# Kernel tuning notes

Hardware: AMD Instinct MI355X
Metric: run time of the kernel (lower is better)

The kernel has to match this reference:

```python
import jax, jax.numpy as jnp
import numpy as np

NOPE, ROPE, LORA, VDIM = 128, 64, 512, 128
T, H, S = 1024, 16, 8192
NUM_CHUNKS = 4  # prefix chunks merged via online-softmax LSE combine
SCALING = (NOPE + ROPE) ** -0.5


def setup_inputs() -> dict:
    key = jax.random.key(0)
    k1, k2, k3, k4 = jax.random.split(key, 4)
    q = jax.random.normal(k1, (T, H, NOPE + ROPE), dtype=jnp.float32)
    kv_cache = jax.random.normal(k2, (S, LORA + ROPE), dtype=jnp.float32)  # latent KV cache [S, 576]
    w_kc = jax.random.normal(k3, (H, NOPE, LORA), dtype=jnp.float32) * (NOPE ** -0.5)
    w_vc = jax.random.normal(k4, (H, LORA, VDIM), dtype=jnp.float32) * (LORA ** -0.5)
    return {"q": q, "kv_cache": kv_cache, "w_kc": w_kc, "w_vc": w_vc}


def _chunk_attn(q_full, kv):
    # q_full: [T,H,576], kv chunk: [C,576] (MQA: single latent KV head)
    scores = jnp.einsum('thd,sd->ths', q_full, kv) * SCALING
    lse = jax.nn.logsumexp(scores, axis=-1)               # [T,H]
    p = jnp.exp(scores - lse[..., None])                  # [T,H,C]
    out = jnp.einsum('ths,sl->thl', p, kv[:, :LORA])      # value = latent kv_lora part
    return out, lse


def reference(q, kv_cache, w_kc, w_vc):
    # --- weight-absorbed query projection (forward_absorb) ---
    q_nope, q_pe = q[..., :NOPE], q[..., NOPE:]
    q_lora = jnp.einsum('thn,hnl->thl', q_nope, w_kc)     # bmm(q_nope^T, w_kc)
    q_full = jnp.concatenate([q_lora, q_pe], axis=-1)     # [T,H,576]

    # --- chunked MQA over latent cache with LSE merge (merge_state_v2) ---
    chunks = kv_cache.reshape(NUM_CHUNKS, S // NUM_CHUNKS, LORA + ROPE)
    acc_out, acc_lse = _chunk_attn(q_full, chunks[0])

    def merge(carry, kv):
        a_out, a_lse = carry
        o, lse = _chunk_attn(q_full, kv)
        new_lse = jnp.logaddexp(a_lse, lse)
        new_out = (a_out * jnp.exp(a_lse - new_lse)[..., None]
                   + o * jnp.exp(lse - new_lse)[..., None])
        return (new_out, new_lse), None

    (attn_out, _), _ = jax.lax.scan(merge, (acc_out, acc_lse), chunks[1:])

    # --- weight-absorbed value projection: bmm(attn^T, w_vc) ---
    out = jnp.einsum('thl,hlv->thv', attn_out, w_vc)      # [T,H,128]
    return out.reshape(T, H * VDIM)
```

## Files before the change

### kernel.cpp

```cpp
#include <hip/hip_runtime.h>
#include <stdint.h>
#include <stddef.h>

#define T_TOK 1024
#define NH    16
#define S_KV  8192
#define DQK   576
#define DV    512
#define NROWS (T_TOK*NH)
#define SCALING 0.072168783648703220563f
#define M_FIX 8.0f

#define SC 32
#define NT (S_KV/SC)
#define KV_CH (72*SC)
#define VT_CH (4*DV)

typedef __attribute__((ext_vector_type(8))) short bf16x8;
typedef __attribute__((ext_vector_type(4))) float f32x4;

__device__ __forceinline__ uint16_t f2bf(float f) {
  uint32_t u = __float_as_uint(f);
  u += 0x7FFFu + ((u >> 16) & 1u);
  return (uint16_t)(u >> 16);
}
__device__ __forceinline__ uint32_t pk2(float a, float b) {
  return (uint32_t)f2bf(a) | ((uint32_t)f2bf(b) << 16);
}
__device__ __forceinline__ void async16(void* lds, const void* g) {
  __builtin_amdgcn_global_load_lds((const __attribute__((address_space(1))) void*)g,
                                   (__attribute__((address_space(3))) void*)lds, 16, 0, 0);
}

__global__ __launch_bounds__(256) void prep_all(
    const float* __restrict__ q, const float* __restrict__ w_kc,
    const float* __restrict__ kv, const float* __restrict__ w_vc,
    uint16_t* __restrict__ q_full, uint16_t* __restrict__ kv_t,
    uint16_t* __restrict__ vt_t, uint16_t* __restrict__ wvt) {
  const int b = blockIdx.x, tid = threadIdx.x;
  __shared__ float qn[32][128];

  if (b < 512) {
    const int h = b >> 5, t0 = (b & 31) * 32;
    #pragma unroll
    for (int r = 0; r < 4; ++r) {
      int idx4 = r * 256 + tid;
      int row = idx4 >> 5, c4 = (idx4 & 31) * 4;
      const float4 v = *(const float4*)(q + ((size_t)((t0 + row) * NH + h)) * 192 + c4);
      *(float4*)&qn[row][c4] = v;
    }
    __syncthreads();
    const int ty = tid >> 6, tx = tid & 63;
    float acc[8][8];
    #pragma unroll
    for (int i = 0; i < 8; ++i)
      #pragma unroll
      for (int j = 0; j < 8; ++j) acc[i][j] = 0.f;
    for (int n = 0; n < 128; ++n) {
      const float4 b0 = *(const float4*)(w_kc + ((size_t)(h * 128 + n)) * 512 + tx * 8);
      const float4 b1 = *(const float4*)(w_kc + ((size_t)(h * 128 + n)) * 512 + tx * 8 + 4);
      #pragma unroll
      for (int i = 0; i < 8; ++i) {
        const float a = qn[ty * 8 + i][n];
        acc[i][0] += a * b0.x; acc[i][1] += a * b0.y; acc[i][2] += a * b0.z; acc[i][3] += a * b0.w;
        acc[i][4] += a * b1.x; acc[i][5] += a * b1.y; acc[i][6] += a * b1.z; acc[i][7] += a * b1.w;
      }
    }
    #pragma unroll
    for (int i = 0; i < 8; ++i) {
      const size_t R = (size_t)(t0 + ty * 8 + i) * NH + h;
      uint4 o;
      o.x = pk2(acc[i][0]*SCALING, acc[i][1]*SCALING);
      o.y = pk2(acc[i][2]*SCALING, acc[i][3]*SCALING);
      o.z = pk2(acc[i][4]*SCALING, acc[i][5]*SCALING);
      o.w = pk2(acc[i][6]*SCALING, acc[i][7]*SCALING);
      *(uint4*)&q_full[R * DQK + tx * 8] = o;
    }
    {
      const int trow = tid >> 3, j0 = (tid & 7) * 8;
      const float* src = q + ((size_t)((t0 + trow) * NH + h)) * 192 + 128 + j0;
      const float4 a = *(const float4*)(src);
      const float4 c = *(const float4*)(src + 4);
      const size_t R = (size_t)(t0 + trow) * NH + h;
      uint4 o;
      o.x = pk2(a.x*SCALING, a.y*SCALING); o.y = pk2(a.z*SCALING, a.w*SCALING);
      o.z = pk2(c.x*SCALING, c.y*SCALING); o.w = pk2(c.z*SCALING, c.w*SCALING);
      *(uint4*)&q_full[R * DQK + 512 + j0] = o;
    }
  } else if (b < 768) {
    const int st = b - 512;
    uint16_t* kvo = kv_t + (size_t)st * (KV_CH * 8);
    #pragma unroll
    for (int r = 0; r < 9; ++r) {
      const int k = r * 256 + tid;
      const int dc = k >> 5, sl = k & 31;
      const float* src = kv + ((size_t)(st * SC + sl)) * DQK + dc * 8;
      const float4 a = *(const float4*)src;
      const float4 c = *(const float4*)(src + 4);
      uint4 o;
      o.x = pk2(a.x, a.y); o.y = pk2(a.z, a.w); o.z = pk2(c.x, c.y); o.w = pk2(c.z, c.w);
      *(uint4*)&kvo[(size_t)k * 8] = o;
    }
    uint16_t* vto = vt_t + (size_t)st * (VT_CH * 8);
    #pragma unroll
    for (int r = 0; r < 8; ++r) {
      const int k = r * 256 + tid;
      const int sc = k >> 9, v = k & 511;
      float val[8];
      #pragma unroll
      for (int e = 0; e < 8; ++e)
        val[e] = kv[((size_t)(st * SC + sc * 8 + e)) * DQK + v];
      uint4 o;
      o.x = pk2(val[0], val[1]); o.y = pk2(val[2], val[3]);
      o.z = pk2(val[4], val[5]); o.w = pk2(val[6], val[7]);
      *(uint4*)&vto[(size_t)k * 8] = o;
    }
  } else {
    const int c = (b - 768) * 256 + tid;
    const int h = c >> 13, rem = c & 8191;
    const int lc = rem >> 7, v = rem & 127;
    const float* src = w_vc + ((size_t)h * 512 + lc * 8) * 128 + v;
    float val[8];
    #pragma unroll
    for (int e = 0; e < 8; ++e) val[e] = src[e * 128];
    uint4 o;
    o.x = pk2(val[0], val[1]); o.y = pk2(val[2], val[3]);
    o.z = pk2(val[4], val[5]); o.w = pk2(val[6], val[7]);
    *(uint4*)&wvt[(size_t)c * 8] = o;
  }
}

__global__ __launch_bounds__(768, 3) void attn_kernel(
    const uint16_t* __restrict__ q_full, const uint16_t* __restrict__ kv_t,
    const uint16_t* __restrict__ vt_t, uint16_t* __restrict__ attn_o) {
  __shared__ short kv_lds[2][KV_CH * 8];
  __shared__ short P_lds[2][260 * 8];
  __shared__ float l_sh[64];

  const int tid = threadIdx.x;
  const int wv = tid >> 6, lane = tid & 63;
  const int cc = lane & 15, quad = lane >> 4;
  const int R0 = blockIdx.x * 64;

  if (wv < 4) {
    const int qh = wv;
    bf16x8 qf[18];
    {
      const uint16_t* qrow = q_full + (size_t)(R0 + 16 * qh + cc) * DQK + quad * 8;
      #pragma unroll
      for (int kk = 0; kk < 18; ++kk)
        qf[kk] = *(const bf16x8*)(qrow + kk * 32);
    }
    const int e = cc & 7, scb = cc >> 3;
    const int qb0 = 16 * qh + quad * 4;

    for (int st = 0; st <= NT; ++st) {
      __syncthreads();
      if (st < NT) {
        const short* kb = kv_lds[st & 1];
        f32x4 sa0 = {0.f,0.f,0.f,0.f}, sa1 = {0.f,0.f,0.f,0.f};
        __builtin_amdgcn_s_setprio(1);
        #pragma unroll
        for (int kk = 0; kk < 18; ++kk) {
          const bf16x8 b0 = *(const bf16x8*)&kb[((kk * 4 + quad) * SC + cc) * 8];
          const bf16x8 b1 = *(const bf16x8*)&kb[((kk * 4 + quad) * SC + 16 + cc) * 8];
          sa0 = __builtin_amdgcn_mfma_f32_16x16x32_bf16(qf[kk], b0, sa0, 0, 0, 0);
          sa1 = __builtin_amdgcn_mfma_f32_16x16x32_bf16(qf[kk], b1, sa1, 0, 0, 0);
        }
        __builtin_amdgcn_s_setprio(0);
        short* Pb = P_lds[st & 1];
        #pragma unroll
        for (int r = 0; r < 4; ++r) {
          Pb[(scb * 65 + qb0 + r) * 8 + e]       = (short)f2bf(__expf(sa0[r] - M_FIX));
          Pb[((2 + scb) * 65 + qb0 + r) * 8 + e] = (short)f2bf(__expf(sa1[r] - M_FIX));
        }
      }
    }
    __syncthreads();
  } else {
    const int ci = wv - 4;
    f32x4 acc[4][4];
    #pragma unroll
    for (int a = 0; a < 4; ++a)
      #pragma unroll
      for (int b = 0; b < 4; ++b) acc[a][b] = (f32x4){0.f, 0.f, 0.f, 0.f};
    f32x4 accl[4];
    #pragma unroll
    for (int a = 0; a < 4; ++a) accl[a] = (f32x4){0.f, 0.f, 0.f, 0.f};
    bf16x8 ones;
    #pragma unroll
    for (int e2 = 0; e2 < 8; ++e2) ones[e2] = (short)0x3F80;

    {
      const uint16_t* kt = kv_t;
      #pragma unroll
      for (int r = 0; r < 5; ++r) {
        const int base = r * 512 + ci * 64;
        if (base < KV_CH)
          async16(&kv_lds[0][base * 8], kt + (size_t)(base + lane) * 8);
      }
    }

    for (int st = 0; st <= NT; ++st) {
      __syncthreads();
      bf16x8 vt4[4];
      if (st > 0) {
        const uint16_t* vtile = vt_t + (size_t)(st - 1) * (VT_CH * 8);
        #pragma unroll
        for (int vj = 0; vj < 4; ++vj)
          vt4[vj] = *(const bf16x8*)(vtile + (size_t)(quad * 512 + 64 * ci + 16 * vj + cc) * 8);
      }
      if (st + 1 < NT) {
        const uint16_t* kt = kv_t + (size_t)(st + 1) * (KV_CH * 8);
        short* dst = kv_lds[(st + 1) & 1];
        #pragma unroll
        for (int r = 0; r < 5; ++r) {
          const int base = r * 512 + ci * 64;
          if (base < KV_CH)
            async16(&dst[base * 8], kt + (size_t)(base + lane) * 8);
        }
      }
      if (st > 0) {
        const short* Pb = P_lds[(st - 1) & 1];
        bf16x8 af[4];
        #pragma unroll
        for (int q2 = 0; q2 < 4; ++q2)
          af[q2] = *(const bf16x8*)&Pb[(quad * 65 + 16 * q2 + cc) * 8];
        __builtin_amdgcn_s_setprio(1);
        if (ci == 0) {
          #pragma unroll
          for (int q2 = 0; q2 < 4; ++q2)
            accl[q2] = __builtin_amdgcn_mfma_f32_16x16x32_bf16(af[q2], ones, accl[q2], 0, 0, 0);
        }
        #pragma unroll
        for (int q2 = 0; q2 < 4; ++q2)
          #pragma unroll
          for (int vj = 0; vj < 4; ++vj)
            acc[q2][vj] = __builtin_amdgcn_mfma_f32_16x16x32_bf16(af[q2], vt4[vj], acc[q2][vj], 0, 0, 0);
        __builtin_amdgcn_s_setprio(0);
      }
    }
    if (ci == 0 && cc == 0) {
      #pragma unroll
      for (int q2 = 0; q2 < 4; ++q2)
        #pragma unroll
        for (int r = 0; r < 4; ++r)
          l_sh[16 * q2 + quad * 4 + r] = accl[q2][r];
    }
    __syncthreads();
    #pragma unroll
    for (int q2 = 0; q2 < 4; ++q2) {
      #pragma unroll
      for (int r = 0; r < 4; ++r) {
        const int row = 16 * q2 + quad * 4 + r;
        const float li = 1.0f / l_sh[row];
        #pragma unroll
        for (int vj = 0; vj < 4; ++vj)
          attn_o[(size_t)(R0 + row) * DV + 64 * ci + 16 * vj + cc] = f2bf(acc[q2][vj][r] * li);
      }
    }
  }
}

__global__ __launch_bounds__(256) void out_proj(const uint16_t* __restrict__ attn_o,
                                                const uint16_t* __restrict__ wvt,
                                                float* __restrict__ out) {
  const int h = blockIdx.y, t0 = blockIdx.x * 64;
  const int wv = threadIdx.x >> 6, lane = threadIdx.x & 63;
  const int cc = lane & 15, quad = lane >> 4;

  f32x4 acc[8];
  #pragma unroll
  for (int vj = 0; vj < 8; ++vj) acc[vj] = (f32x4){0.f, 0.f, 0.f, 0.f};

  const uint16_t* arow = attn_o + ((size_t)(t0 + wv * 16 + cc) * NH + h) * DV + quad * 8;
  const uint16_t* wb = wvt + (size_t)h * (64 * 128) * 8;
  #pragma unroll 4
  for (int kk = 0; kk < 16; ++kk) {
    const bf16x8 a = *(const bf16x8*)(arow + kk * 32);
    #pragma unroll
    for (int vj = 0; vj < 8; ++vj) {
      const bf16x8 b = *(const bf16x8*)(wb + (size_t)(((kk * 4 + quad) * 128) + 16 * vj + cc) * 8);
      acc[vj] = __builtin_amdgcn_mfma_f32_16x16x32_bf16(a, b, acc[vj], 0, 0, 0);
    }
  }
  #pragma unroll
  for (int vj = 0; vj < 8; ++vj)
    #pragma unroll
    for (int r = 0; r < 4; ++r)
      out[(size_t)(t0 + wv * 16 + quad * 4 + r) * (NH * 128) + h * 128 + 16 * vj + cc] = acc[vj][r];
}

extern "C" void kernel_launch(void* const* d_in, const int* in_sizes, int n_in,
                              void* d_out, int out_size, void* d_ws, size_t ws_size,
                              hipStream_t stream) {
  const float* q    = (const float*)d_in[0];
  const float* kv   = (const float*)d_in[1];
  const float* w_kc = (const float*)d_in[2];
  const float* w_vc = (const float*)d_in[3];
  float* out = (float*)d_out;

  char* ws = (char*)d_ws;
  const size_t SZ_QF = (size_t)NROWS * DQK * 2;
  const size_t SZ_KT = (size_t)NT * KV_CH * 16;
  const size_t SZ_VT = (size_t)NT * VT_CH * 16;
  const size_t SZ_AO = (size_t)NROWS * DV * 2;
  uint16_t* q_full = (uint16_t*)(ws);
  uint16_t* kv_t   = (uint16_t*)(ws + SZ_QF);
  uint16_t* vt_t   = (uint16_t*)(ws + SZ_QF + SZ_KT);
  uint16_t* attn_o = (uint16_t*)(ws + SZ_QF + SZ_KT + SZ_VT);
  uint16_t* wvt    = (uint16_t*)(ws + SZ_QF + SZ_KT + SZ_VT + SZ_AO);

  prep_all<<<1280, 256, 0, stream>>>(q, w_kc, kv, w_vc, q_full, kv_t, vt_t, wvt);
  attn_kernel<<<256, 768, 0, stream>>>(q_full, kv_t, vt_t, attn_o);
  out_proj<<<dim3(16, 16), 256, 0, stream>>>(attn_o, wvt, out);
}
```

Baseline: 415.0 us.

## Split QK^T across waves along the reduction dimension with LDS partial-sum exchange

The four score waves now each cover 32 query rows and half of the 576-wide reduction instead of 16 rows and the full reduction. Each B fragment read from LDS is reused across two query tiles, which halves per-wave LDS reads of the KV tile. One wave of each pair writes its fp32 partial sums to a new shared buffer, and the other adds them in the next stage before the exp and bf16 store to P. This adds a pipeline stage that delays the PV consumers by one step, plus extra shared memory and LDS traffic for the partials. It also concentrates the exp work on half the score waves.

```diff
diff --git a/kernel.cpp b/kernel.cpp
--- a/kernel.cpp
+++ b/kernel.cpp
@@ -135,6 +135,7 @@
     const uint16_t* __restrict__ vt_t, uint16_t* __restrict__ attn_o) {
   __shared__ short kv_lds[2][KV_CH * 8];
   __shared__ short P_lds[2][260 * 8];
+  __shared__ float S_part[2][2][2][2][16][20];
   __shared__ float l_sh[64];
 
   const int tid = threadIdx.x;
@@ -143,36 +144,60 @@
   const int R0 = blockIdx.x * 64;
 
   if (wv < 4) {
-    const int qh = wv;
-    bf16x8 qf[18];
-    {
-      const uint16_t* qrow = q_full + (size_t)(R0 + 16 * qh + cc) * DQK + quad * 8;
-      #pragma unroll
-      for (int kk = 0; kk < 18; ++kk)
-        qf[kk] = *(const bf16x8*)(qrow + kk * 32);
+    const int kh = wv >> 1, qg = wv & 1;
+    bf16x8 qf[2][9];
+    #pragma unroll
+    for (int qt = 0; qt < 2; ++qt) {
+      const uint16_t* qrow = q_full + (size_t)(R0 + qg * 32 + qt * 16 + cc) * DQK + quad * 8;
+      #pragma unroll
+      for (int j = 0; j < 9; ++j)
+        qf[qt][j] = *(const bf16x8*)(qrow + (kh * 9 + j) * 32);
     }
     const int e = cc & 7, scb = cc >> 3;
-    const int qb0 = 16 * qh + quad * 4;
-
-    for (int st = 0; st <= NT; ++st) {
+    f32x4 sa[2][2];
+
+    for (int st = 0; st <= NT + 1; ++st) {
       __syncthreads();
+      if (kh == 0 && st >= 1 && st <= NT) {
+        short* Pb = P_lds[(st - 1) & 1];
+        const int pb = (st - 1) & 1;
+        #pragma unroll
+        for (int qt = 0; qt < 2; ++qt)
+          #pragma unroll
+          for (int sh = 0; sh < 2; ++sh) {
+            const f32x4 part = *(const f32x4*)&S_part[pb][qg][qt][sh][cc][quad * 4];
+            const int qb = qg * 32 + qt * 16 + quad * 4;
+            const int sc = 2 * sh + scb;
+            #pragma unroll
+            for (int r = 0; r < 4; ++r)
+              Pb[(sc * 65 + qb + r) * 8 + e] =
+                  (short)f2bf(__expf(sa[qt][sh][r] + part[r] - M_FIX));
+          }
+      }
       if (st < NT) {
         const short* kb = kv_lds[st & 1];
-        f32x4 sa0 = {0.f,0.f,0.f,0.f}, sa1 = {0.f,0.f,0.f,0.f};
+        #pragma unroll
+        for (int qt = 0; qt < 2; ++qt)
+          #pragma unroll
+          for (int sh = 0; sh < 2; ++sh) sa[qt][sh] = (f32x4){0.f, 0.f, 0.f, 0.f};
         __builtin_amdgcn_s_setprio(1);
         #pragma unroll
-        for (int kk = 0; kk < 18; ++kk) {
+        for (int j = 0; j < 9; ++j) {
+          const int kk = kh * 9 + j;
           const bf16x8 b0 = *(const bf16x8*)&kb[((kk * 4 + quad) * SC + cc) * 8];
           const bf16x8 b1 = *(const bf16x8*)&kb[((kk * 4 + quad) * SC + 16 + cc) * 8];
-          sa0 = __builtin_amdgcn_mfma_f32_16x16x32_bf16(qf[kk], b0, sa0, 0, 0, 0);
-          sa1 = __builtin_amdgcn_mfma_f32_16x16x32_bf16(qf[kk], b1, sa1, 0, 0, 0);
+          sa[0][0] = __builtin_amdgcn_mfma_f32_16x16x32_bf16(qf[0][j], b0, sa[0][0], 0, 0, 0);
+          sa[0][1] = __builtin_amdgcn_mfma_f32_16x16x32_bf16(qf[0][j], b1, sa[0][1], 0, 0, 0);
+          sa[1][0] = __builtin_amdgcn_mfma_f32_16x16x32_bf16(qf[1][j], b0, sa[1][0], 0, 0, 0);
+          sa[1][1] = __builtin_amdgcn_mfma_f32_16x16x32_bf16(qf[1][j], b1, sa[1][1], 0, 0, 0);
         }
         __builtin_amdgcn_s_setprio(0);
-        short* Pb = P_lds[st & 1];
-        #pragma unroll
-        for (int r = 0; r < 4; ++r) {
-          Pb[(scb * 65 + qb0 + r) * 8 + e]       = (short)f2bf(__expf(sa0[r] - M_FIX));
-          Pb[((2 + scb) * 65 + qb0 + r) * 8 + e] = (short)f2bf(__expf(sa1[r] - M_FIX));
+        if (kh == 1) {
+          #pragma unroll
+          for (int qt = 0; qt < 2; ++qt)
+            #pragma unroll
+            for (int sh = 0; sh < 2; ++sh)
+              *(f32x4*)&S_part[st & 1][qg][qt][sh][cc][quad * 4] = sa[qt][sh];
         }
       }
     }
@@ -201,11 +226,11 @@
       }
     }
 
-    for (int st = 0; st <= NT; ++st) {
+    for (int st = 0; st <= NT + 1; ++st) {
       __syncthreads();
       bf16x8 vt4[4];
-      if (st > 0) {
-        const uint16_t* vtile = vt_t + (size_t)(st - 1) * (VT_CH * 8);
+      if (st >= 2) {
+        const uint16_t* vtile = vt_t + (size_t)(st - 2) * (VT_CH * 8);
         #pragma unroll
         for (int vj = 0; vj < 4; ++vj)
           vt4[vj] = *(const bf16x8*)(vtile + (size_t)(quad * 512 + 64 * ci + 16 * vj + cc) * 8);
@@ -220,8 +245,8 @@
             async16(&dst[base * 8], kt + (size_t)(base + lane) * 8);
         }
       }
-      if (st > 0) {
-        const short* Pb = P_lds[(st - 1) & 1];
+      if (st >= 2) {
+        const short* Pb = P_lds[(st - 2) & 1];
         bf16x8 af[4];
         #pragma unroll
         for (int q2 = 0; q2 < 4; ++q2)
```

After: 450.4 us. 8.5% more time.
